# Performance work log

Hardware: AMD Instinct MI355X
Metric: run time of the kernel (lower is better)

Reference implementation:

```python
import jax, jax.numpy as jnp
import numpy as np

B, T, D, U = 8, 1024, 128, 2048
LEAK = 0.5       # leak_rate
EXPONENT = 2     # PowerIndex exponent
POW_INDEX = 2    # square neurons whose index % POW_INDEX == 0


def setup_inputs() -> dict:
    key = jax.random.key(0)
    k1, k2, k3, k4 = jax.random.split(key, 4)
    inputs = jax.random.normal(k1, (B, T, D), dtype=jnp.float32)
    # input-to-reservoir weights (InputMatrix ~ scaled dense here)
    w_in = jax.random.normal(k2, (D, U), dtype=jnp.float32) * (1.0 / np.sqrt(D))
    b_in = jax.random.uniform(k3, (U,), dtype=jnp.float32, minval=-0.05, maxval=0.05)
    # reservoir kernel (ErdosRenyi sparse random; dense surrogate scaled to
    # spectral radius ~0.9 via 0.9/sqrt(U))
    w_res = jax.random.normal(k4, (U, U), dtype=jnp.float32) * (0.9 / np.sqrt(U))
    return {"inputs": inputs, "w_in": w_in, "b_in": b_in, "w_res": w_res}


def reference(inputs, w_in, b_in, w_res):
    # Leaky ESN recurrence scanned over time:
    a = jnp.asarray(LEAK, inputs.dtype)
    # Precompute the input projection for all timesteps in one big GEMM.
    proj = jnp.einsum('btd,du->btu', inputs, w_in) + b_in  # [B,T,U]

    def step(state, p_t):  # state: [B,U], p_t: [B,U]
        pre = p_t + state @ w_res
        new = (1.0 - a) * state + a * jnp.tanh(pre)
        return new, new

    s0 = jnp.zeros((inputs.shape[0], w_res.shape[0]), inputs.dtype)
    _, states = jax.lax.scan(step, s0, jnp.swapaxes(proj, 0, 1))  # [T,B,U]
    states = jnp.swapaxes(states, 0, 1)  # [B,T,U]

    # PowerIndex: raise neurons at every POW_INDEX-th position to EXPONENT
    idx = jnp.arange(states.shape[-1])
    powered = jnp.where(idx % POW_INDEX == 0, states ** EXPONENT, states)

    # raw=False: concat input with reservoir output along features
    return jnp.concatenate([inputs, powered], axis=-1)  # [B,T,D+U]
```

## Files before the change

### kernel.cpp

```cpp
#include <hip/hip_runtime.h>
#include <cmath>

typedef __attribute__((ext_vector_type(8))) short short8;
typedef __attribute__((ext_vector_type(4))) float f32x4;
typedef unsigned long long u64;
typedef unsigned int u32;

#define RS 2208

__device__ __forceinline__ unsigned short f2bf(float x){
  u32 u = __float_as_uint(x);
  u32 r = u + 0x7FFFu + ((u >> 16) & 1u);
  return (unsigned short)(r >> 16);
}

__device__ __forceinline__ float tanh_fast(float x){
  float xc = fminf(fmaxf(x, -10.f), 10.f);
  float e = __expf(2.f * xc);
  return (e - 1.f) / (e + 1.f);
}

__global__ void bswz_kernel(const float* __restrict__ wres,
                            const float* __restrict__ win,
                            unsigned short* __restrict__ B){
  int tid = blockIdx.x * 256 + threadIdx.x;
  int l   = tid & 63;
  int cf  = tid >> 6;
  int f   = cf % 34;
  int gk  = cf / 34;
  int ks  = gk & 1;
  int gcg = gk >> 1;
  int col = (gcg << 4) + (l & 15);
  int k0  = ks * 1088 + (f << 5) + ((l >> 4) << 3);
  short8 vv;
  #pragma unroll
  for (int j = 0; j < 8; ++j){
    int k = k0 + j;
    float v = (k < 2048) ? wres[(size_t)k * 2048 + col]
                         : win[(size_t)(k - 2048) * 2048 + col];
    vv[j] = (short)f2bf(v);
  }
  *((short8*)(B + (size_t)tid * 8)) = vv;
}

__global__ void copy_in_kernel(const float* __restrict__ in, float* __restrict__ out){
  int i = blockIdx.x * 256 + threadIdx.x;
  int bt = i >> 5;
  int d4 = i & 31;
  float4 v = ((const float4*)in)[i];
  ((float4*)(out + (size_t)bt * 2176))[d4] = v;
}

__global__ void exinit_kernel(u64* __restrict__ ex){
  int i = blockIdx.x * 256 + threadIdx.x;
  ex[i] = (i < 4096) ? 0ULL : 0x0001000100010001ULL;
}

__global__ void __launch_bounds__(512, 2) esn_persist(
    const float* __restrict__ inputs,
    const float* __restrict__ b_in,
    const unsigned short* __restrict__ Bsw,
    u64* __restrict__ ex,
    float* __restrict__ out)
{
  __shared__ __align__(16) unsigned short As[2 * RS];
  __shared__ float red[2][4][16][2];

  const int tid = threadIdx.x;
  const int blk = blockIdx.x;
  const int r0  = (blk >> 5) << 1;
  const int cb  = blk & 31;
  const int wv  = tid >> 6;
  const int l   = tid & 63;
  const int m16 = l & 15;
  const int q   = l >> 4;
  const int cg  = wv >> 1;
  const int ks  = wv & 1;
  const int gcg = (cb << 2) + cg;
  const int colw0 = gcg << 4;

  short8 Bf[34];
  {
    const short8* bp = (const short8*)Bsw + (size_t)((gcg << 1) + ks) * 34 * 64 + l;
    #pragma unroll
    for (int f = 0; f < 34; ++f) Bf[f] = bp[f * 64];
  }
  const float bias = b_in[colw0 + m16];
  float s0 = 0.f, s1 = 0.f;

  const float* xr0 = inputs + (size_t)r0 * 1024 * 128;
  const u64 M = 0x0001000100010001ULL;

  for (int t = 0; t < 1024; ++t){
    if (tid < 64){
      const int row = tid >> 5;
      const int c   = tid & 31;
      float4 xv = ((const float4*)(xr0 + ((size_t)row * 1024 + t) * 128))[c];
      u64 pk = (u64)f2bf(xv.x) | ((u64)f2bf(xv.y) << 16)
             | ((u64)f2bf(xv.z) << 32) | ((u64)f2bf(xv.w) << 48);
      *((u64*)&As[row * RS + 2048 + (c << 2)]) = pk;
    }
    {
      u64* srcb = ex + ((size_t)(t & 1) * 8 + r0) * 512;
      const u64 wantm = ((t >> 1) & 1) ? M : 0ULL;
      u64 v0 = __hip_atomic_load(&srcb[tid],       __ATOMIC_RELAXED, __HIP_MEMORY_SCOPE_AGENT);
      u64 v1 = __hip_atomic_load(&srcb[512 + tid], __ATOMIC_RELAXED, __HIP_MEMORY_SCOPE_AGENT);
      u32 pend = 3;
      while (pend){
        u32 np = 0;
        if (pend & 1){
          if ((v0 & M) == wantm) *((u64*)&As[tid << 2]) = v0;
          else np |= 1;
        }
        if (pend & 2){
          if ((v1 & M) == wantm) *((u64*)&As[RS + (tid << 2)]) = v1;
          else np |= 2;
        }
        pend = np;
        if (pend & 1) v0 = __hip_atomic_load(&srcb[tid],       __ATOMIC_RELAXED, __HIP_MEMORY_SCOPE_AGENT);
        if (pend & 2) v1 = __hip_atomic_load(&srcb[512 + tid], __ATOMIC_RELAXED, __HIP_MEMORY_SCOPE_AGENT);
      }
    }
    __syncthreads();

    f32x4 acc0 = {0.f,0.f,0.f,0.f}, acc1 = {0.f,0.f,0.f,0.f};
    {
      const unsigned short* Ab = &As[(m16 & 1) * RS + ks * 1088 + (q << 3)];
      #pragma unroll
      for (int f = 0; f < 34; f += 2){
        short8 a0 = *((const short8*)(Ab + (f << 5)));
        short8 a1 = *((const short8*)(Ab + ((f + 1) << 5)));
        acc0 = __builtin_amdgcn_mfma_f32_16x16x32_bf16(a0, Bf[f],     acc0, 0, 0, 0);
        acc1 = __builtin_amdgcn_mfma_f32_16x16x32_bf16(a1, Bf[f + 1], acc1, 0, 0, 0);
      }
    }
    float p0 = acc0[0] + acc1[0];
    float p1 = acc0[1] + acc1[1];
    if (ks == 1 && l < 16){
      red[t & 1][cg][m16][0] = p0;
      red[t & 1][cg][m16][1] = p1;
    }
    __syncthreads();

    if (ks == 0 && l < 16){
      p0 += red[t & 1][cg][m16][0];
      p1 += red[t & 1][cg][m16][1];
      float nv0 = 0.5f * s0 + 0.5f * tanh_fast(p0 + bias);
      float nv1 = 0.5f * s1 + 0.5f * tanh_fast(p1 + bias);
      s0 = nv0; s1 = nv1;
      const u32 bit = (u32)(((t + 1) >> 1) & 1);
      u32 b0 = ((u32)f2bf(nv0) & 0xFFFEu) | bit;
      u32 b1 = ((u32)f2bf(nv1) & 0xFFFEu) | bit;
      u32 pr0 = b0 | (((u32)__shfl_xor((int)b0, 1)) << 16);
      u32 pr1 = b1 | (((u32)__shfl_xor((int)b1, 1)) << 16);
      u64 e0 = (u64)pr0 | ((u64)(u32)__shfl_xor((int)pr0, 2) << 32);
      u64 e1 = (u64)pr1 | ((u64)(u32)__shfl_xor((int)pr1, 2) << 32);
      const int u = colw0 + m16;
      if ((m16 & 3) == 0){
        u64* exw = ex + ((size_t)((t + 1) & 1) * 8 + r0) * 512;
        const int p = (colw0 + m16) >> 2;
        __hip_atomic_store(&exw[p],       e0, __ATOMIC_RELAXED, __HIP_MEMORY_SCOPE_AGENT);
        __hip_atomic_store(&exw[512 + p], e1, __ATOMIC_RELAXED, __HIP_MEMORY_SCOPE_AGENT);
      }
      float pw0 = (u & 1) ? nv0 : nv0 * nv0;
      float pw1 = (u & 1) ? nv1 : nv1 * nv1;
      out[((size_t)r0 * 1024 + t) * 2176 + 128 + u] = pw0;
      out[((size_t)(r0 + 1) * 1024 + t) * 2176 + 128 + u] = pw1;
    }
  }
}

extern "C" void kernel_launch(void* const* d_in, const int* in_sizes, int n_in,
                              void* d_out, int out_size, void* d_ws, size_t ws_size,
                              hipStream_t stream){
  const float* inputs = (const float*)d_in[0];
  const float* w_in   = (const float*)d_in[1];
  const float* b_in   = (const float*)d_in[2];
  const float* w_res  = (const float*)d_in[3];
  float* out = (float*)d_out;

  u64* ex = (u64*)d_ws;
  unsigned short* Bsw = (unsigned short*)((char*)d_ws + 65536);

  exinit_kernel<<<32, 256, 0, stream>>>(ex);
  bswz_kernel<<<2176, 256, 0, stream>>>(w_res, w_in, Bsw);
  copy_in_kernel<<<1024, 256, 0, stream>>>(inputs, out);
  esn_persist<<<128, 512, 0, stream>>>(inputs, b_in, Bsw, ex, out);
}
```

Before: 3.123 ms.

## Add per-batch-row wide persistent ESN kernel with co-residency check and fallback

Adds a new persistent kernel that gives each block a single batch row and a full 2176-deep K slice per wave, dropping the cross-wave shared-memory reduction and the second __syncthreads per timestep. Global exchange now goes through inline-asm sc0 loads and stores. A startup handshake uses realtime-clock timeouts to confirm that all 256 blocks are co-resident, and if that fails the old kernel runs as a fallback. The wider layout doubles register use for the B fragments and spreads the work over 256 blocks, which relies on all of them being resident at once. The spin guard can also break out and write stale values, a correctness risk.

```diff
diff --git a/kernel.cpp b/kernel.cpp
--- a/kernel.cpp
+++ b/kernel.cpp
@@ -7,6 +7,8 @@
 typedef unsigned int u32;
 
 #define RS 2208
+#define TICKS_MS 100000ull
+#define SCAN_SPIN (1u << 18)
 
 __device__ __forceinline__ unsigned short f2bf(float x){
   u32 u = __float_as_uint(x);
@@ -18,6 +20,24 @@
   float xc = fminf(fmaxf(x, -10.f), 10.f);
   float e = __expf(2.f * xc);
   return (e - 1.f) / (e + 1.f);
+}
+
+__device__ __forceinline__ u64 rtc(){ return __builtin_amdgcn_s_memrealtime(); }
+
+__device__ __forceinline__ u64 ld_sc0(const u64* p){
+  u64 v;
+  asm volatile("global_load_dwordx2 %0, %1, off sc0\n\ts_waitcnt vmcnt(0)"
+               : "=v"(v) : "v"(p) : "memory");
+  return v;
+}
+__device__ __forceinline__ void st_sc0(u64* p, u64 v){
+  asm volatile("global_store_dwordx2 %0, %1, off sc0" :: "v"(p), "v"(v) : "memory");
+}
+__device__ __forceinline__ void ld2_sc0(const u64* p0, const u64* p1, u64& a, u64& b){
+  asm volatile("global_load_dwordx2 %0, %2, off sc0\n\t"
+               "global_load_dwordx2 %1, %3, off sc0\n\t"
+               "s_waitcnt vmcnt(0)"
+               : "=&v"(a), "=&v"(b) : "v"(p0), "v"(p1) : "memory");
 }
 
 __global__ void bswz_kernel(const float* __restrict__ wres,
@@ -53,10 +73,148 @@
 
 __global__ void exinit_kernel(u64* __restrict__ ex){
   int i = blockIdx.x * 256 + threadIdx.x;
-  ex[i] = (i < 4096) ? 0ULL : 0x0001000100010001ULL;
-}
-
-__global__ void __launch_bounds__(512, 2) esn_persist(
+  if (i < 8192)      ex[i] = (i < 4096) ? 0ULL : 0x0001000100010001ULL;
+  else if (i < 8704) ex[i] = 0ULL;
+}
+
+__global__ void __launch_bounds__(256, 1) esn_wide(
+    const float* __restrict__ inputs,
+    const float* __restrict__ b_in,
+    const unsigned short* __restrict__ Bsw,
+    u64* __restrict__ ex,
+    float* __restrict__ out)
+{
+  __shared__ __align__(16) unsigned short As[2][2176];
+  __shared__ int sflag;
+
+  const int tid = threadIdx.x;
+  const int blk = blockIdx.x;
+  const int r   = blk & 7;
+  const int cb  = blk >> 3;
+  u32* ctrl   = (u32*)(ex + 8192);
+  u64* tslots = ex + 8192 + 8;
+
+  if (tid == 0){
+    __hip_atomic_fetch_add(&ctrl[0], 1u, __ATOMIC_RELAXED, __HIP_MEMORY_SCOPE_AGENT);
+    const int partner = (((cb + 1) & 31) << 3) | r;
+    int ok = 1;
+    for (int rd = 1; rd <= 4 && ok; ++rd){
+      st_sc0(&tslots[blk], (u64)rd);
+      u64 tend = rtc() + TICKS_MS;
+      u64 v;
+      do { v = ld_sc0(&tslots[partner]); } while (v < (u64)rd && rtc() < tend);
+      ok = (v >= (u64)rd) ? 1 : 0;
+    }
+    if (ok) __hip_atomic_fetch_add(&ctrl[1], 1u, __ATOMIC_RELAXED, __HIP_MEMORY_SCOPE_AGENT);
+    if (blk == 0){
+      u64 tend = rtc() + 3 * TICKS_MS;
+      u32 c, o;
+      do {
+        c = __hip_atomic_load(&ctrl[0], __ATOMIC_RELAXED, __HIP_MEMORY_SCOPE_AGENT);
+        o = __hip_atomic_load(&ctrl[1], __ATOMIC_RELAXED, __HIP_MEMORY_SCOPE_AGENT);
+      } while (!(c == 256u && o == 256u) && rtc() < tend);
+      __hip_atomic_store(&ctrl[2], (c == 256u && o == 256u) ? 1u : 2u,
+                         __ATOMIC_RELAXED, __HIP_MEMORY_SCOPE_AGENT);
+    }
+    u64 tend = rtc() + 12 * TICKS_MS;
+    u32 v;
+    do { v = __hip_atomic_load(&ctrl[2], __ATOMIC_RELAXED, __HIP_MEMORY_SCOPE_AGENT); }
+    while (v == 0u && rtc() < tend);
+    sflag = (v == 1u);
+  }
+  __syncthreads();
+  if (!sflag) return;
+
+  const int w   = tid >> 6;
+  const int l   = tid & 63;
+  const int m16 = l & 15;
+  const int q   = l >> 4;
+  const int gcg = (cb << 2) + w;
+  const int colw0 = gcg << 4;
+
+  short8 Bf[68];
+  {
+    const short8* bp = (const short8*)Bsw + (size_t)gcg * (68 * 64) + l;
+    #pragma unroll
+    for (int f = 0; f < 68; ++f) Bf[f] = bp[f * 64];
+  }
+  const float bias = b_in[colw0 + m16];
+  float s = 0.f;
+  const float* xr = inputs + (size_t)r * 1024 * 128;
+  const u64 M = 0x0001000100010001ULL;
+
+  float4 xv;
+  if (tid < 32) xv = ((const float4*)xr)[tid];
+
+  for (int t = 0; t < 1024; ++t){
+    const int p = t & 1;
+    unsigned short* Ap = &As[p][0];
+
+    if (tid < 32){
+      u64 pk = (u64)f2bf(xv.x) | ((u64)f2bf(xv.y) << 16)
+             | ((u64)f2bf(xv.z) << 32) | ((u64)f2bf(xv.w) << 48);
+      *((u64*)&Ap[2048 + (tid << 2)]) = pk;
+      if (t < 1023) xv = ((const float4*)(xr + (size_t)(t + 1) * 128))[tid];
+    }
+    {
+      u64* srcb = ex + ((size_t)p * 8 + r) * 512;
+      const u64 want = ((t >> 1) & 1) ? M : 0ULL;
+      u64 v0, v1;
+      ld2_sc0(&srcb[tid], &srcb[tid + 256], v0, v1);
+      u32 pend = 3, guard = 0;
+      while (pend){
+        u32 np = 0;
+        if (pend & 1){ if ((v0 & M) == want) *((u64*)&Ap[tid << 2]) = v0; else np |= 1; }
+        if (pend & 2){ if ((v1 & M) == want) *((u64*)&Ap[(tid + 256) << 2]) = v1; else np |= 2; }
+        pend = np;
+        if (pend){
+          if (++guard > SCAN_SPIN){
+            if (pend & 1) *((u64*)&Ap[tid << 2]) = v0;
+            if (pend & 2) *((u64*)&Ap[(tid + 256) << 2]) = v1;
+            break;
+          }
+          if (pend & 1) v0 = ld_sc0(&srcb[tid]);
+          if (pend & 2) v1 = ld_sc0(&srcb[tid + 256]);
+        }
+      }
+    }
+    __syncthreads();
+
+    f32x4 a0 = {0,0,0,0}, a1 = {0,0,0,0}, a2 = {0,0,0,0}, a3 = {0,0,0,0};
+    {
+      const unsigned short* Ab = Ap + (q << 3);
+      #pragma unroll
+      for (int f = 0; f < 68; f += 4){
+        short8 x0 = *((const short8*)(Ab + ((f + 0) << 5)));
+        short8 x1 = *((const short8*)(Ab + ((f + 1) << 5)));
+        short8 x2 = *((const short8*)(Ab + ((f + 2) << 5)));
+        short8 x3 = *((const short8*)(Ab + ((f + 3) << 5)));
+        a0 = __builtin_amdgcn_mfma_f32_16x16x32_bf16(x0, Bf[f + 0], a0, 0, 0, 0);
+        a1 = __builtin_amdgcn_mfma_f32_16x16x32_bf16(x1, Bf[f + 1], a1, 0, 0, 0);
+        a2 = __builtin_amdgcn_mfma_f32_16x16x32_bf16(x2, Bf[f + 2], a2, 0, 0, 0);
+        a3 = __builtin_amdgcn_mfma_f32_16x16x32_bf16(x3, Bf[f + 3], a3, 0, 0, 0);
+      }
+    }
+    if (l < 16){
+      float pre = ((a0[0] + a1[0]) + (a2[0] + a3[0])) + bias;
+      float nv = 0.5f * s + 0.5f * tanh_fast(pre);
+      s = nv;
+      const u32 bit = (u32)(((t + 1) >> 1) & 1);
+      u32 b0 = ((u32)f2bf(nv) & 0xFFFEu) | bit;
+      u32 pr = b0 | (((u32)__shfl_xor((int)b0, 1)) << 16);
+      u64 e  = (u64)pr | ((u64)(u32)__shfl_xor((int)pr, 2) << 32);
+      if ((m16 & 3) == 0){
+        u64* exw = ex + ((size_t)((t + 1) & 1) * 8 + r) * 512;
+        st_sc0(&exw[(colw0 + m16) >> 2], e);
+      }
+      const int u = colw0 + m16;
+      float pw = (u & 1) ? nv : nv * nv;
+      out[((size_t)r * 1024 + t) * 2176 + 128 + u] = pw;
+    }
+  }
+}
+
+__global__ void __launch_bounds__(512, 2) esn_safe(
     const float* __restrict__ inputs,
     const float* __restrict__ b_in,
     const unsigned short* __restrict__ Bsw,
@@ -65,6 +223,12 @@
 {
   __shared__ __align__(16) unsigned short As[2 * RS];
   __shared__ float red[2][4][16][2];
+  __shared__ int g;
+
+  if (threadIdx.x == 0)
+    g = (int)__hip_atomic_load(&((u32*)(ex + 8192))[2], __ATOMIC_RELAXED, __HIP_MEMORY_SCOPE_AGENT);
+  __syncthreads();
+  if (g == 1) return;
 
   const int tid = threadIdx.x;
   const int blk = blockIdx.x;
@@ -180,10 +344,11 @@
   float* out = (float*)d_out;
 
   u64* ex = (u64*)d_ws;
-  unsigned short* Bsw = (unsigned short*)((char*)d_ws + 65536);
-
-  exinit_kernel<<<32, 256, 0, stream>>>(ex);
+  unsigned short* Bsw = (unsigned short*)((char*)d_ws + 69632);
+
+  exinit_kernel<<<34, 256, 0, stream>>>(ex);
   bswz_kernel<<<2176, 256, 0, stream>>>(w_res, w_in, Bsw);
   copy_in_kernel<<<1024, 256, 0, stream>>>(inputs, out);
-  esn_persist<<<128, 512, 0, stream>>>(inputs, b_in, Bsw, ex, out);
-}
+  esn_wide<<<256, 256, 0, stream>>>(inputs, b_in, Bsw, ex, out);
+  esn_safe<<<128, 512, 0, stream>>>(inputs, b_in, Bsw, ex, out);
+}
```

Result: slower. 7.160 ms (+129.2%).

## Split K four ways with 1024-thread blocks and prefetch next input row

Applied to the files above, without the earlier changes.

Doubles the threads per block to 1024 and splits each column group's K dimension across four waves instead of two. This halves the MFMA chain and register-resident B fragments per wave, and the partial sums are reduced through a larger shared-memory buffer. Each thread now polls a single exchange word instead of two, and the next timestep's input row is prefetched into registers. The risks are lower occupancy per CU and a heavier reduction step and barrier cost with more waves.

```diff
diff --git a/kernel.cpp b/kernel.cpp
--- a/kernel.cpp
+++ b/kernel.cpp
@@ -7,6 +7,7 @@
 typedef unsigned int u32;
 
 #define RS 2208
+#define AG __ATOMIC_RELAXED, __HIP_MEMORY_SCOPE_AGENT
 
 __device__ __forceinline__ unsigned short f2bf(float x){
   u32 u = __float_as_uint(x);
@@ -56,7 +57,7 @@
   ex[i] = (i < 4096) ? 0ULL : 0x0001000100010001ULL;
 }
 
-__global__ void __launch_bounds__(512, 2) esn_persist(
+__global__ void __launch_bounds__(1024) esn_persist(
     const float* __restrict__ inputs,
     const float* __restrict__ b_in,
     const unsigned short* __restrict__ Bsw,
@@ -64,7 +65,7 @@
     float* __restrict__ out)
 {
   __shared__ __align__(16) unsigned short As[2 * RS];
-  __shared__ float red[2][4][16][2];
+  __shared__ float red[2][3][4][16][2];
 
   const int tid = threadIdx.x;
   const int blk = blockIdx.x;
@@ -74,16 +75,16 @@
   const int l   = tid & 63;
   const int m16 = l & 15;
   const int q   = l >> 4;
-  const int cg  = wv >> 1;
-  const int ks  = wv & 1;
+  const int cg  = wv >> 2;
+  const int ks  = wv & 3;
   const int gcg = (cb << 2) + cg;
   const int colw0 = gcg << 4;
 
-  short8 Bf[34];
+  short8 Bf[17];
   {
-    const short8* bp = (const short8*)Bsw + (size_t)((gcg << 1) + ks) * 34 * 64 + l;
+    const short8* bp = (const short8*)Bsw + (size_t)(gcg * 68 + ks * 17) * 64 + l;
     #pragma unroll
-    for (int f = 0; f < 34; ++f) Bf[f] = bp[f * 64];
+    for (int f = 0; f < 17; ++f) Bf[f] = bp[f * 64];
   }
   const float bias = b_in[colw0 + m16];
   float s0 = 0.f, s1 = 0.f;
@@ -91,60 +92,52 @@
   const float* xr0 = inputs + (size_t)r0 * 1024 * 128;
   const u64 M = 0x0001000100010001ULL;
 
+  float4 xv;
+  if (tid < 64) xv = ((const float4*)(xr0 + (size_t)(tid >> 5) * 1024 * 128))[tid & 31];
+
   for (int t = 0; t < 1024; ++t){
     if (tid < 64){
       const int row = tid >> 5;
       const int c   = tid & 31;
-      float4 xv = ((const float4*)(xr0 + ((size_t)row * 1024 + t) * 128))[c];
       u64 pk = (u64)f2bf(xv.x) | ((u64)f2bf(xv.y) << 16)
              | ((u64)f2bf(xv.z) << 32) | ((u64)f2bf(xv.w) << 48);
       *((u64*)&As[row * RS + 2048 + (c << 2)]) = pk;
+      if (t < 1023)
+        xv = ((const float4*)(xr0 + ((size_t)row * 1024 + t + 1) * 128))[c];
     }
     {
       u64* srcb = ex + ((size_t)(t & 1) * 8 + r0) * 512;
-      const u64 wantm = ((t >> 1) & 1) ? M : 0ULL;
-      u64 v0 = __hip_atomic_load(&srcb[tid],       __ATOMIC_RELAXED, __HIP_MEMORY_SCOPE_AGENT);
-      u64 v1 = __hip_atomic_load(&srcb[512 + tid], __ATOMIC_RELAXED, __HIP_MEMORY_SCOPE_AGENT);
-      u32 pend = 3;
-      while (pend){
-        u32 np = 0;
-        if (pend & 1){
-          if ((v0 & M) == wantm) *((u64*)&As[tid << 2]) = v0;
-          else np |= 1;
-        }
-        if (pend & 2){
-          if ((v1 & M) == wantm) *((u64*)&As[RS + (tid << 2)]) = v1;
-          else np |= 2;
-        }
-        pend = np;
-        if (pend & 1) v0 = __hip_atomic_load(&srcb[tid],       __ATOMIC_RELAXED, __HIP_MEMORY_SCOPE_AGENT);
-        if (pend & 2) v1 = __hip_atomic_load(&srcb[512 + tid], __ATOMIC_RELAXED, __HIP_MEMORY_SCOPE_AGENT);
-      }
+      const u64 want = ((t >> 1) & 1) ? M : 0ULL;
+      u64 v = __hip_atomic_load(&srcb[tid], AG);
+      while ((v & M) != want) v = __hip_atomic_load(&srcb[tid], AG);
+      *((u64*)&As[(tid >> 9) * RS + ((tid & 511) << 2)]) = v;
     }
     __syncthreads();
 
     f32x4 acc0 = {0.f,0.f,0.f,0.f}, acc1 = {0.f,0.f,0.f,0.f};
     {
-      const unsigned short* Ab = &As[(m16 & 1) * RS + ks * 1088 + (q << 3)];
+      const unsigned short* Ab = &As[(m16 & 1) * RS + ks * 544 + (q << 3)];
       #pragma unroll
-      for (int f = 0; f < 34; f += 2){
+      for (int f = 0; f < 16; f += 2){
         short8 a0 = *((const short8*)(Ab + (f << 5)));
         short8 a1 = *((const short8*)(Ab + ((f + 1) << 5)));
         acc0 = __builtin_amdgcn_mfma_f32_16x16x32_bf16(a0, Bf[f],     acc0, 0, 0, 0);
         acc1 = __builtin_amdgcn_mfma_f32_16x16x32_bf16(a1, Bf[f + 1], acc1, 0, 0, 0);
       }
+      short8 a2 = *((const short8*)(Ab + (16 << 5)));
+      acc0 = __builtin_amdgcn_mfma_f32_16x16x32_bf16(a2, Bf[16], acc0, 0, 0, 0);
     }
     float p0 = acc0[0] + acc1[0];
     float p1 = acc0[1] + acc1[1];
-    if (ks == 1 && l < 16){
-      red[t & 1][cg][m16][0] = p0;
-      red[t & 1][cg][m16][1] = p1;
+    if (ks != 0 && l < 16){
+      red[t & 1][ks - 1][cg][m16][0] = p0;
+      red[t & 1][ks - 1][cg][m16][1] = p1;
     }
     __syncthreads();
 
     if (ks == 0 && l < 16){
-      p0 += red[t & 1][cg][m16][0];
-      p1 += red[t & 1][cg][m16][1];
+      p0 += red[t & 1][0][cg][m16][0] + red[t & 1][1][cg][m16][0] + red[t & 1][2][cg][m16][0];
+      p1 += red[t & 1][0][cg][m16][1] + red[t & 1][1][cg][m16][1] + red[t & 1][2][cg][m16][1];
       float nv0 = 0.5f * s0 + 0.5f * tanh_fast(p0 + bias);
       float nv1 = 0.5f * s1 + 0.5f * tanh_fast(p1 + bias);
       s0 = nv0; s1 = nv1;
@@ -159,8 +152,8 @@
       if ((m16 & 3) == 0){
         u64* exw = ex + ((size_t)((t + 1) & 1) * 8 + r0) * 512;
         const int p = (colw0 + m16) >> 2;
-        __hip_atomic_store(&exw[p],       e0, __ATOMIC_RELAXED, __HIP_MEMORY_SCOPE_AGENT);
-        __hip_atomic_store(&exw[512 + p], e1, __ATOMIC_RELAXED, __HIP_MEMORY_SCOPE_AGENT);
+        __hip_atomic_store(&exw[p],       e0, AG);
+        __hip_atomic_store(&exw[512 + p], e1, AG);
       }
       float pw0 = (u & 1) ? nv0 : nv0 * nv0;
       float pw1 = (u & 1) ? nv1 : nv1 * nv1;
@@ -185,5 +178,5 @@
   exinit_kernel<<<32, 256, 0, stream>>>(ex);
   bswz_kernel<<<2176, 256, 0, stream>>>(w_res, w_in, Bsw);
   copy_in_kernel<<<1024, 256, 0, stream>>>(inputs, out);
-  esn_persist<<<128, 512, 0, stream>>>(inputs, b_in, Bsw, ex, out);
+  esn_persist<<<128, 1024, 0, stream>>>(inputs, b_in, Bsw, ex, out);
 }
```

Result: slower. 3.398 ms (+8.8%).

## Vectorize cross-block state polling, use atomic exchange publish, prefetch next input row

Applied to the files above, without the earlier changes.

Each thread now polls two adjacent exchange words with a single 128-bit coherent load (sc0 sc1) and retries until both carry the expected parity. Every eighth retry falls back to regular atomic loads. After that it writes both words contiguously into shared memory. Producers publish state with atomic exchange instead of relaxed atomic store, so the write is pushed to the coherent level sooner. The per-step input row load is software-prefetched one step ahead. Together these aim to cut the latency of the per-timestep inter-block handoff, at the cost of inline asm and a wider wait condition.

```diff
diff --git a/kernel.cpp b/kernel.cpp
--- a/kernel.cpp
+++ b/kernel.cpp
@@ -3,10 +3,12 @@
 
 typedef __attribute__((ext_vector_type(8))) short short8;
 typedef __attribute__((ext_vector_type(4))) float f32x4;
+typedef __attribute__((ext_vector_type(4))) unsigned int u32x4;
 typedef unsigned long long u64;
 typedef unsigned int u32;
 
 #define RS 2208
+#define AG __ATOMIC_RELAXED, __HIP_MEMORY_SCOPE_AGENT
 
 __device__ __forceinline__ unsigned short f2bf(float x){
   u32 u = __float_as_uint(x);
@@ -91,35 +93,43 @@
   const float* xr0 = inputs + (size_t)r0 * 1024 * 128;
   const u64 M = 0x0001000100010001ULL;
 
+  float4 xv;
+  if (tid < 64) xv = ((const float4*)(xr0 + (size_t)(tid >> 5) * 1024 * 128))[tid & 31];
+
   for (int t = 0; t < 1024; ++t){
     if (tid < 64){
       const int row = tid >> 5;
       const int c   = tid & 31;
-      float4 xv = ((const float4*)(xr0 + ((size_t)row * 1024 + t) * 128))[c];
       u64 pk = (u64)f2bf(xv.x) | ((u64)f2bf(xv.y) << 16)
              | ((u64)f2bf(xv.z) << 32) | ((u64)f2bf(xv.w) << 48);
       *((u64*)&As[row * RS + 2048 + (c << 2)]) = pk;
+      if (t < 1023)
+        xv = ((const float4*)(xr0 + ((size_t)row * 1024 + t + 1) * 128))[c];
     }
     {
       u64* srcb = ex + ((size_t)(t & 1) * 8 + r0) * 512;
-      const u64 wantm = ((t >> 1) & 1) ? M : 0ULL;
-      u64 v0 = __hip_atomic_load(&srcb[tid],       __ATOMIC_RELAXED, __HIP_MEMORY_SCOPE_AGENT);
-      u64 v1 = __hip_atomic_load(&srcb[512 + tid], __ATOMIC_RELAXED, __HIP_MEMORY_SCOPE_AGENT);
-      u32 pend = 3;
-      while (pend){
-        u32 np = 0;
-        if (pend & 1){
-          if ((v0 & M) == wantm) *((u64*)&As[tid << 2]) = v0;
-          else np |= 1;
+      const u64 want = ((t >> 1) & 1) ? M : 0ULL;
+      const u64* myp = &srcb[tid << 1];
+      u64 v0, v1;
+      u32 it = 0;
+      for (;;){
+        if ((it & 7u) == 7u){
+          v0 = __hip_atomic_load(&myp[0], AG);
+          v1 = __hip_atomic_load(&myp[1], AG);
+        } else {
+          u32x4 v;
+          asm volatile("global_load_dwordx4 %0, %1, off sc0 sc1\n\ts_waitcnt vmcnt(0)"
+                       : "=v"(v) : "v"(myp) : "memory");
+          v0 = (u64)v.x | ((u64)v.y << 32);
+          v1 = (u64)v.z | ((u64)v.w << 32);
         }
-        if (pend & 2){
-          if ((v1 & M) == wantm) *((u64*)&As[RS + (tid << 2)]) = v1;
-          else np |= 2;
-        }
-        pend = np;
-        if (pend & 1) v0 = __hip_atomic_load(&srcb[tid],       __ATOMIC_RELAXED, __HIP_MEMORY_SCOPE_AGENT);
-        if (pend & 2) v1 = __hip_atomic_load(&srcb[512 + tid], __ATOMIC_RELAXED, __HIP_MEMORY_SCOPE_AGENT);
+        if (((v0 & M) == want) && ((v1 & M) == want)) break;
+        ++it;
       }
+      const int row = tid >> 8;
+      const int e   = tid & 255;
+      u64* dst = (u64*)&As[row * RS + (e << 3)];
+      dst[0] = v0; dst[1] = v1;
     }
     __syncthreads();
 
@@ -159,8 +169,8 @@
       if ((m16 & 3) == 0){
         u64* exw = ex + ((size_t)((t + 1) & 1) * 8 + r0) * 512;
         const int p = (colw0 + m16) >> 2;
-        __hip_atomic_store(&exw[p],       e0, __ATOMIC_RELAXED, __HIP_MEMORY_SCOPE_AGENT);
-        __hip_atomic_store(&exw[512 + p], e1, __ATOMIC_RELAXED, __HIP_MEMORY_SCOPE_AGENT);
+        (void)__hip_atomic_exchange(&exw[p],       e0, AG);
+        (void)__hip_atomic_exchange(&exw[512 + p], e1, AG);
       }
       float pw0 = (u & 1) ? nv0 : nv0 * nv0;
       float pw1 = (u & 1) ? nv1 : nv1 * nv1;
```

Result: no change. 3.117 ms (-0.2%).
